# Kernel optimization log

Hardware: AMD Instinct MI355X
Metric: run time of the kernel (lower is better)

The kernel has to match this reference:

```python
import jax, jax.numpy as jnp
import numpy as np

B, T, D_MODEL = 1, 2048, 2048
N_HEADS, N_KV_HEADS, HEAD_DIM = 32, 8, 64
N_REP = N_HEADS // N_KV_HEADS
ROPE_THETA = 10000.0


def setup_inputs() -> dict:
    key = jax.random.key(0)
    ks = jax.random.split(key, 5)
    x = jax.random.normal(ks[0], (B, T, D_MODEL), dtype=jnp.float32)
    # rotary frequencies: complex exp stored as (cos, sin) pairs -> [T, HEAD_DIM//2, 2]
    inv_freq = 1.0 / (ROPE_THETA ** (jnp.arange(0, HEAD_DIM, 2, dtype=jnp.float32) / HEAD_DIM))
    angles = jnp.arange(T, dtype=jnp.float32)[:, None] * inv_freq[None, :]  # [T, HEAD_DIM//2]
    freqs_cis = jnp.stack([jnp.cos(angles), jnp.sin(angles)], axis=-1)  # [T, HD/2, 2]
    s = 1.0 / np.sqrt(D_MODEL)
    wq = jax.random.normal(ks[1], (D_MODEL, N_HEADS * HEAD_DIM), dtype=jnp.float32) * s
    wk = jax.random.normal(ks[2], (D_MODEL, N_KV_HEADS * HEAD_DIM), dtype=jnp.float32) * s
    wv = jax.random.normal(ks[3], (D_MODEL, N_KV_HEADS * HEAD_DIM), dtype=jnp.float32) * s
    wo = jax.random.normal(ks[4], (N_HEADS * HEAD_DIM, D_MODEL), dtype=jnp.float32) * (1.0 / np.sqrt(N_HEADS * HEAD_DIM))
    return {"x": x, "freqs_cis": freqs_cis, "wq": wq, "wk": wk, "wv": wv, "wo": wo}


def _apply_rotary(t, freqs_cis):
    # t: [B, T, H, D]; freqs_cis: [T, D//2, 2] as (cos, sin). Complex multiply.
    tr = t.astype(jnp.float32).reshape(*t.shape[:-1], -1, 2)  # [B,T,H,D/2,2]
    re, im = tr[..., 0], tr[..., 1]
    cos = freqs_cis[None, :, None, :, 0]  # [1,T,1,D/2]
    sin = freqs_cis[None, :, None, :, 1]
    out_re = re * cos - im * sin
    out_im = re * sin + im * cos
    out = jnp.stack([out_re, out_im], axis=-1).reshape(t.shape)
    return out.astype(t.dtype)


def reference(x, freqs_cis, wq, wk, wv, wo):
    Bx, Tx, _ = x.shape
    q = (x @ wq).reshape(Bx, Tx, N_HEADS, HEAD_DIM)
    k = (x @ wk).reshape(Bx, Tx, N_KV_HEADS, HEAD_DIM)
    v = (x @ wv).reshape(Bx, Tx, N_KV_HEADS, HEAD_DIM)
    q = _apply_rotary(q, freqs_cis)
    k = _apply_rotary(k, freqs_cis)
    # GQA: group query heads, broadcast against kv heads (no repeat materialization)
    qg = q.transpose(0, 2, 1, 3).reshape(Bx, N_KV_HEADS, N_REP, Tx, HEAD_DIM)  # [B,G,R,T,D]
    kg = k.transpose(0, 2, 1, 3)  # [B,G,T,D]
    vg = v.transpose(0, 2, 1, 3)  # [B,G,T,D]
    scale = 1.0 / np.sqrt(HEAD_DIM)
    scores = jnp.einsum('bgrtd,bgsd->bgrts', qg, kg) * scale  # [B,G,R,T,T]
    causal = jnp.tril(jnp.ones((Tx, Tx), dtype=bool))
    scores = jnp.where(causal, scores, jnp.finfo(scores.dtype).min)
    p = jax.nn.softmax(scores, axis=-1)
    y = jnp.einsum('bgrts,bgsd->bgrtd', p, vg)  # [B,G,R,T,D]
    y = y.reshape(Bx, N_HEADS, Tx, HEAD_DIM).transpose(0, 2, 1, 3).reshape(Bx, Tx, N_HEADS * HEAD_DIM)
    return y @ wo
```

## Files before the change

### kernel.cpp

```cpp
#include <hip/hip_runtime.h>
#include <hip/hip_bf16.h>
#include <stdint.h>
#include <stddef.h>

#define T_SEQ 2048
#define DMODEL 2048
#define NHEADS 32
#define NKV 8
#define HD 64
#define NQD (NHEADS * HD)
#define NKVD (NKV * HD)
#define QKVN (NQD + 2 * NKVD)

typedef __bf16 bf16_t;
typedef __bf16 bf16x8 __attribute__((ext_vector_type(8)));
typedef __bf16 bf16x4 __attribute__((ext_vector_type(4)));
typedef __bf16 bf16x2 __attribute__((ext_vector_type(2)));
typedef float f32x4 __attribute__((ext_vector_type(4)));

typedef __attribute__((address_space(1))) void gvoid_t;
typedef __attribute__((address_space(3))) void lvoid_t;

__device__ __forceinline__ void gload_lds16(const void* g, void* l) {
  __builtin_amdgcn_global_load_lds((gvoid_t*)g, (lvoid_t*)l, 16, 0, 0);
}

__global__ __launch_bounds__(256) void cast_f32_bf16_kernel(
    const float* __restrict__ in, bf16_t* __restrict__ out, int n8) {
  int i = blockIdx.x * 256 + threadIdx.x;
  if (i >= n8) return;
  const float4* p = (const float4*)in + (size_t)i * 2;
  float4 a = p[0], b = p[1];
  bf16x8 o = {(bf16_t)a.x, (bf16_t)a.y, (bf16_t)a.z, (bf16_t)a.w,
              (bf16_t)b.x, (bf16_t)b.y, (bf16_t)b.z, (bf16_t)b.w};
  *(bf16x8*)(out + (size_t)i * 8) = o;
}

__global__ __launch_bounds__(256) void transpose_cast_kernel(
    const float* __restrict__ in, bf16_t* __restrict__ out,
    int R, int C, int ldin, int ldout) {
  __shared__ float tile[32][33];
  const int c0 = blockIdx.x * 32, r0 = blockIdx.y * 32;
  const int tx = threadIdx.x & 31, ty = threadIdx.x >> 5;
#pragma unroll
  for (int i = 0; i < 32; i += 8)
    tile[ty + i][tx] = in[(size_t)(r0 + ty + i) * ldin + c0 + tx];
  __syncthreads();
#pragma unroll
  for (int i = 0; i < 32; i += 8)
    out[(size_t)(c0 + ty + i) * ldout + r0 + tx] = (bf16_t)tile[tx][ty + i];
}

__global__ __launch_bounds__(256) void rope_cast_kernel(
    const float* __restrict__ src, const float* __restrict__ fc,
    bf16_t* __restrict__ dst, int H, int ldin, float oscale) {
  const int i = blockIdx.x * 256 + threadIdx.x;
  const int npr = H * 32;
  const int t = i / npr;
  const int rem = i - t * npr;
  const int h = rem >> 5, fi = rem & 31;
  const float2 rein = *(const float2*)&src[(size_t)t * ldin + h * 64 + fi * 2];
  const float2 cs = *(const float2*)&fc[((size_t)t * 32 + fi) * 2];
  const float o0 = (rein.x * cs.x - rein.y * cs.y) * oscale;
  const float o1 = (rein.x * cs.y + rein.y * cs.x) * oscale;
  bf16x2 ob = {(bf16_t)o0, (bf16_t)o1};
  *(bf16x2*)&dst[(size_t)t * (H * 64) + h * 64 + fi * 2] = ob;
}

__global__ __launch_bounds__(256) void gemm_bt64_kernel(
    const bf16_t* __restrict__ A, const bf16_t* __restrict__ BT,
    float* __restrict__ C, int M, int N, int K) {
  __shared__ bf16_t As[128 * 64];
  __shared__ bf16_t Bs[64 * 64];
  const int tid = threadIdx.x;
  const int lane = tid & 63;
  const int w = tid >> 6;
  const int lr = lane & 15, lg = lane >> 4;
  const int m0 = blockIdx.y * 128, n0 = blockIdx.x * 64;
  const int wm = (w >> 1) * 64, wn = (w & 1) * 32;

  const bf16_t* gA[4];
  bf16_t* lA[4];
#pragma unroll
  for (int j = 0; j < 4; ++j) {
    const int c = tid + j * 256;
    const int row = c >> 3, cc = c & 7;
    gA[j] = A + (size_t)(m0 + row) * K + ((cc ^ (row & 7)) * 8);
    lA[j] = As + c * 8;
  }
  const bf16_t* gB[2];
  bf16_t* lB[2];
#pragma unroll
  for (int j = 0; j < 2; ++j) {
    const int c = tid + j * 256;
    const int row = c >> 3, cc = c & 7;
    gB[j] = BT + (size_t)(n0 + row) * K + ((cc ^ (row & 7)) * 8);
    lB[j] = Bs + c * 8;
  }

  f32x4 acc[4][2] = {};

  for (int k0 = 0; k0 < K; k0 += 64) {
#pragma unroll
    for (int j = 0; j < 4; ++j) gload_lds16(gA[j] + k0, lA[j]);
#pragma unroll
    for (int j = 0; j < 2; ++j) gload_lds16(gB[j] + k0, lB[j]);
    __syncthreads();
#pragma unroll
    for (int ks = 0; ks < 2; ++ks) {
      bf16x8 af[4], bfr[2];
#pragma unroll
      for (int mi = 0; mi < 4; ++mi) {
        const int row = wm + mi * 16 + lr;
        af[mi] = *(const bf16x8*)((const char*)As + row * 128 +
                                  ((ks * 64 + lg * 16) ^ ((row & 7) << 4)));
      }
#pragma unroll
      for (int nj = 0; nj < 2; ++nj) {
        const int row = wn + nj * 16 + lr;
        bfr[nj] = *(const bf16x8*)((const char*)Bs + row * 128 +
                                   ((ks * 64 + lg * 16) ^ ((row & 7) << 4)));
      }
      __builtin_amdgcn_s_setprio(1);
#pragma unroll
      for (int mi = 0; mi < 4; ++mi)
#pragma unroll
        for (int nj = 0; nj < 2; ++nj)
          acc[mi][nj] = __builtin_amdgcn_mfma_f32_16x16x32_bf16(
              af[mi], bfr[nj], acc[mi][nj], 0, 0, 0);
      __builtin_amdgcn_s_setprio(0);
    }
    __syncthreads();
  }

#pragma unroll
  for (int mi = 0; mi < 4; ++mi)
#pragma unroll
    for (int nj = 0; nj < 2; ++nj) {
      const int row = m0 + wm + mi * 16 + lg * 4;
      const int col = n0 + wn + nj * 16 + lr;
#pragma unroll
      for (int r = 0; r < 4; ++r)
        C[(size_t)(row + r) * N + col] = acc[mi][nj][r];
    }
}

__global__ __launch_bounds__(256) void attn_kernel(
    const bf16_t* __restrict__ Q, const bf16_t* __restrict__ Kb,
    const bf16_t* __restrict__ VT, bf16_t* __restrict__ Y,
    bf16_t* __restrict__ Yp, float* __restrict__ Mb, float* __restrict__ Lb) {
  __shared__ bf16_t Ks[2][64 * 64];
  __shared__ char Pb[4][32 * 128];
  const int bid = blockIdx.x;
  const int kh = bid & 7;
  const int item = bid >> 3;
  int qt, c, nc;
  if (item < 75) { qt = 63 - item / 3; c = item % 3; nc = 3; }
  else if (item < 115) { const int j = item - 75; qt = 38 - (j >> 1); c = j & 1; nc = 2; }
  else { qt = 18 - (item - 115); c = 0; nc = 1; }
  const int nt = (qt + 2) >> 1;
  const int tstart = (nt * c) / nc;
  const int tend = (nt * (c + 1)) / nc;
  const bool single = (nc == 1);

  const int tid = threadIdx.x, lane = tid & 63, w = tid >> 6;
  const int h = kh * 4 + w;
  const int lr = lane & 15, lg = lane >> 4;
  const int q0 = qt * 32;
  char* pb = (char*)Pb[w];
  const int swz = (lr & 7) << 4;

  const int r1 = tid >> 3, cc1 = tid & 7;
  const int r2 = r1 + 32;
  const bf16_t* kg1 = Kb + (size_t)r1 * NKVD + kh * HD + ((cc1 ^ (r1 & 7)) * 8);
  const bf16_t* kg2 = Kb + (size_t)r2 * NKVD + kh * HD + ((cc1 ^ (r2 & 7)) * 8);
  const int ld1 = tid * 8, ld2 = tid * 8 + 2048;
  const size_t kstep = (size_t)64 * NKVD;

  const bf16_t* vp0 = VT + (size_t)(kh * HD + 0 + lr) * T_SEQ + lg * 8 + tstart * 64;
  const bf16_t* vp1 = VT + (size_t)(kh * HD + 16 + lr) * T_SEQ + lg * 8 + tstart * 64;
  const bf16_t* vp2 = VT + (size_t)(kh * HD + 32 + lr) * T_SEQ + lg * 8 + tstart * 64;
  const bf16_t* vp3 = VT + (size_t)(kh * HD + 48 + lr) * T_SEQ + lg * 8 + tstart * 64;

  bf16x8 qf[2][2];
#pragma unroll
  for (int iq = 0; iq < 2; ++iq)
#pragma unroll
    for (int ks = 0; ks < 2; ++ks)
      qf[iq][ks] = *(const bf16x8*)&Q[(size_t)(q0 + iq * 16 + lr) * NQD + h * HD + ks * 32 + lg * 8];

  float m_i[2] = {-1e30f, -1e30f}, l_i[2] = {0.f, 0.f};
  f32x4 acc_o[2][4] = {};
  const f32x4 Z = {0.f, 0.f, 0.f, 0.f};

  size_t koff = (size_t)tstart * kstep;
  gload_lds16(kg1 + koff, &Ks[0][ld1]);
  gload_lds16(kg2 + koff, &Ks[0][ld2]);
  __syncthreads();

  int cur = 0;
  for (int t = tstart; t < tend; ++t) {
    const int s0 = t * 64;
    if (t + 1 < tend) {
      gload_lds16(kg1 + koff + kstep, &Ks[cur ^ 1][ld1]);
      gload_lds16(kg2 + koff + kstep, &Ks[cur ^ 1][ld2]);
    }
    koff += kstep;

    bf16x8 vf[2][4];
#pragma unroll
    for (int ks = 0; ks < 2; ++ks) {
      vf[ks][0] = *(const bf16x8*)(vp0 + ks * 32);
      vf[ks][1] = *(const bf16x8*)(vp1 + ks * 32);
      vf[ks][2] = *(const bf16x8*)(vp2 + ks * 32);
      vf[ks][3] = *(const bf16x8*)(vp3 + ks * 32);
    }
    vp0 += 64; vp1 += 64; vp2 += 64; vp3 += 64;

    const char* kbase = (const char*)&Ks[cur][0];
    bf16x8 kf[4][2];
#pragma unroll
    for (int j = 0; j < 4; ++j)
#pragma unroll
      for (int ks = 0; ks < 2; ++ks)
        kf[j][ks] = *(const bf16x8*)(kbase + (j * 16 + lr) * 128 + ((ks * 64 + lg * 16) ^ swz));

    f32x4 st[2][4];
    __builtin_amdgcn_s_setprio(1);
#pragma unroll
    for (int iq = 0; iq < 2; ++iq)
#pragma unroll
      for (int j = 0; j < 4; ++j) {
        st[iq][j] = __builtin_amdgcn_mfma_f32_16x16x32_bf16(kf[j][0], qf[iq][0], Z, 0, 0, 0);
        st[iq][j] = __builtin_amdgcn_mfma_f32_16x16x32_bf16(kf[j][1], qf[iq][1], st[iq][j], 0, 0, 0);
      }
    __builtin_amdgcn_s_setprio(0);

    const bool domask = (s0 + 64 > q0);
#pragma unroll
    for (int iq = 0; iq < 2; ++iq) {
      float sv[16];
      const int tq = q0 + iq * 16 + lr;
#pragma unroll
      for (int j = 0; j < 4; ++j)
#pragma unroll
        for (int r = 0; r < 4; ++r) {
          float v = st[iq][j][r];
          if (domask && (s0 + j * 16 + lg * 4 + r > tq)) v = -1e30f;
          sv[j * 4 + r] = v;
        }
      float pm = fmaxf(fmaxf(fmaxf(sv[0], sv[1]), fmaxf(sv[2], sv[3])),
                       fmaxf(fmaxf(sv[4], sv[5]), fmaxf(sv[6], sv[7])));
      float pm2 = fmaxf(fmaxf(fmaxf(sv[8], sv[9]), fmaxf(sv[10], sv[11])),
                        fmaxf(fmaxf(sv[12], sv[13]), fmaxf(sv[14], sv[15])));
      pm = fmaxf(pm, pm2);
      pm = fmaxf(pm, __shfl_xor(pm, 16));
      pm = fmaxf(pm, __shfl_xor(pm, 32));

      if (!__all(pm <= m_i[iq] + 8.0f)) {
        const float mnew = fmaxf(m_i[iq], pm);
        const float es = exp2f(m_i[iq] - mnew);
        m_i[iq] = mnew;
        l_i[iq] *= es;
        float eso[4];
#pragma unroll
        for (int r = 0; r < 4; ++r) eso[r] = __shfl(es, lg * 4 + r);
#pragma unroll
        for (int df = 0; df < 4; ++df)
#pragma unroll
          for (int r = 0; r < 4; ++r) acc_o[iq][df][r] *= eso[r];
      }

      float rs0 = 0.f, rs1 = 0.f;
      bf16_t pe[16];
#pragma unroll
      for (int z = 0; z < 8; ++z) {
        const float p = exp2f(sv[z] - m_i[iq]);
        rs0 += p;
        pe[z] = (bf16_t)p;
      }
#pragma unroll
      for (int z = 8; z < 16; ++z) {
        const float p = exp2f(sv[z] - m_i[iq]);
        rs1 += p;
        pe[z] = (bf16_t)p;
      }
      l_i[iq] += rs0 + rs1;

#pragma unroll
      for (int j = 0; j < 4; ++j) {
        bf16x4 pk = {pe[j * 4 + 0], pe[j * 4 + 1], pe[j * 4 + 2], pe[j * 4 + 3]};
        *(bf16x4*)(pb + (iq * 16 + lr) * 128 + ((j * 32 + lg * 8) ^ swz)) = pk;
      }
    }

    bf16x8 pa[2][2];
#pragma unroll
    for (int iq = 0; iq < 2; ++iq)
#pragma unroll
      for (int ks = 0; ks < 2; ++ks)
        pa[iq][ks] = *(const bf16x8*)(pb + (iq * 16 + lr) * 128 + ((ks * 64 + lg * 16) ^ swz));

    __builtin_amdgcn_s_setprio(1);
#pragma unroll
    for (int iq = 0; iq < 2; ++iq)
#pragma unroll
      for (int df = 0; df < 4; ++df)
#pragma unroll
        for (int ks = 0; ks < 2; ++ks)
          acc_o[iq][df] = __builtin_amdgcn_mfma_f32_16x16x32_bf16(pa[iq][ks], vf[ks][df], acc_o[iq][df], 0, 0, 0);
    __builtin_amdgcn_s_setprio(0);

    __syncthreads();
    cur ^= 1;
  }

  float lts[2];
#pragma unroll
  for (int iq = 0; iq < 2; ++iq) {
    float lt = l_i[iq];
    lt += __shfl_xor(lt, 16);
    lt += __shfl_xor(lt, 32);
    lts[iq] = lt;
  }
  if (single) {
#pragma unroll
    for (int iq = 0; iq < 2; ++iq) {
      float lf[4];
#pragma unroll
      for (int r = 0; r < 4; ++r) lf[r] = __shfl(lts[iq], lg * 4 + r);
#pragma unroll
      for (int r = 0; r < 4; ++r) {
        const float inv = 1.f / lf[r];
        const int t = q0 + iq * 16 + lg * 4 + r;
#pragma unroll
        for (int df = 0; df < 4; ++df)
          Y[(size_t)t * NQD + h * HD + df * 16 + lr] = (bf16_t)(acc_o[iq][df][r] * inv);
      }
    }
  } else {
    const int cid = (nc == 3) ? (kh * 115 + 40 + (qt - 39) * 3 + c)
                              : (kh * 115 + (qt - 19) * 2 + c);
    bf16_t* yp = Yp + ((size_t)cid * 4 + w) * 2048;
#pragma unroll
    for (int iq = 0; iq < 2; ++iq) {
      float lf[4];
#pragma unroll
      for (int r = 0; r < 4; ++r) lf[r] = __shfl(lts[iq], lg * 4 + r);
#pragma unroll
      for (int r = 0; r < 4; ++r) {
        const float inv = 1.f / lf[r];
        const int q = iq * 16 + lg * 4 + r;
#pragma unroll
        for (int df = 0; df < 4; ++df)
          yp[q * 64 + df * 16 + lr] = (bf16_t)(acc_o[iq][df][r] * inv);
      }
    }
    if (lg == 0) {
#pragma unroll
      for (int iq = 0; iq < 2; ++iq) {
        Mb[cid * 128 + w * 32 + iq * 16 + lr] = m_i[iq];
        Lb[cid * 128 + w * 32 + iq * 16 + lr] = lts[iq];
      }
    }
  }
}

__global__ __launch_bounds__(256) void merge_kernel(
    const bf16_t* __restrict__ Yp, const float* __restrict__ Mb,
    const float* __restrict__ Lb, bf16_t* __restrict__ Y) {
  const int qt = 19 + blockIdx.x, kh = blockIdx.y;
  const int w = threadIdx.x >> 6, lane = threadIdx.x & 63;
  const int h = kh * 4 + w;
  const int nc = (qt < 39) ? 2 : 3;
  const int base = (qt < 39) ? (kh * 115 + (qt - 19) * 2)
                             : (kh * 115 + 40 + (qt - 39) * 3);
  const bf16_t* y0 = Yp + ((size_t)(base + 0) * 4 + w) * 2048;
  const bf16_t* y1 = Yp + ((size_t)(base + 1) * 4 + w) * 2048;
  const bf16_t* y2 = Yp + ((size_t)(base + 2) * 4 + w) * 2048;
#pragma unroll 4
  for (int q = 0; q < 32; ++q) {
    const float m0 = Mb[(base + 0) * 128 + w * 32 + q];
    const float m1 = Mb[(base + 1) * 128 + w * 32 + q];
    const float l0 = Lb[(base + 0) * 128 + w * 32 + q];
    const float l1 = Lb[(base + 1) * 128 + w * 32 + q];
    float m2 = -1e30f, l2 = 0.f;
    if (nc == 3) {
      m2 = Mb[(base + 2) * 128 + w * 32 + q];
      l2 = Lb[(base + 2) * 128 + w * 32 + q];
    }
    const float M = fmaxf(fmaxf(m0, m1), m2);
    const float a0 = exp2f(m0 - M) * l0;
    const float a1 = exp2f(m1 - M) * l1;
    const float a2 = (nc == 3) ? exp2f(m2 - M) * l2 : 0.f;
    const float inv = 1.f / (a0 + a1 + a2);
    float v = (float)y0[q * 64 + lane] * a0 + (float)y1[q * 64 + lane] * a1;
    if (nc == 3) v += (float)y2[q * 64 + lane] * a2;
    Y[(size_t)(qt * 32 + q) * NQD + h * HD + lane] = (bf16_t)(v * inv);
  }
}

extern "C" void kernel_launch(void* const* d_in, const int* in_sizes, int n_in,
                              void* d_out, int out_size, void* d_ws, size_t ws_size,
                              hipStream_t stream) {
  const float* x = (const float*)d_in[0];
  const float* fc = (const float*)d_in[1];
  const float* wq = (const float*)d_in[2];
  const float* wk = (const float*)d_in[3];
  const float* wv = (const float*)d_in[4];
  const float* wo = (const float*)d_in[5];
  float* out = (float*)d_out;
  char* ws = (char*)d_ws;

  bf16_t* xb   = (bf16_t*)(ws + 0);
  bf16_t* wT   = (bf16_t*)(ws + (8u << 20));
  float*  qkvf = (float*)(ws + (20u << 20));
  bf16_t* qb   = (bf16_t*)(ws + (8u << 20));
  bf16_t* kb   = (bf16_t*)(ws + (16u << 20));
  bf16_t* vt   = (bf16_t*)(ws + (18u << 20));
  bf16_t* woT  = (bf16_t*)(ws + (20u << 20));
  bf16_t* yb   = (bf16_t*)(ws + 0);
  float*  Mb   = (float*)(ws + (28u << 20));
  float*  Lb   = (float*)(ws + (29u << 20));
  bf16_t* Yp   = (bf16_t*)d_out;

  const float SCL_Q = 0.18033688011112042f;

  hipLaunchKernelGGL(cast_f32_bf16_kernel, dim3(2048), dim3(256), 0, stream,
                     x, xb, (T_SEQ * DMODEL) / 8);
  hipLaunchKernelGGL(transpose_cast_kernel, dim3(64, 64), dim3(256), 0, stream,
                     wq, wT, DMODEL, NQD, NQD, DMODEL);
  hipLaunchKernelGGL(transpose_cast_kernel, dim3(16, 64), dim3(256), 0, stream,
                     wk, wT + (size_t)NQD * DMODEL, DMODEL, NKVD, NKVD, DMODEL);
  hipLaunchKernelGGL(transpose_cast_kernel, dim3(16, 64), dim3(256), 0, stream,
                     wv, wT + (size_t)(NQD + NKVD) * DMODEL, DMODEL, NKVD, NKVD, DMODEL);
  hipLaunchKernelGGL(gemm_bt64_kernel, dim3(QKVN / 64, T_SEQ / 128), dim3(256), 0, stream,
                     xb, wT, qkvf, T_SEQ, QKVN, DMODEL);
  hipLaunchKernelGGL(rope_cast_kernel, dim3((T_SEQ * NHEADS * 32) / 256), dim3(256), 0, stream,
                     qkvf, fc, qb, NHEADS, QKVN, SCL_Q);
  hipLaunchKernelGGL(rope_cast_kernel, dim3((T_SEQ * NKV * 32) / 256), dim3(256), 0, stream,
                     qkvf + NQD, fc, kb, NKV, QKVN, 1.0f);
  hipLaunchKernelGGL(transpose_cast_kernel, dim3(16, 64), dim3(256), 0, stream,
                     qkvf + NQD + NKVD, vt, T_SEQ, NKVD, QKVN, T_SEQ);
  hipLaunchKernelGGL(transpose_cast_kernel, dim3(64, 64), dim3(256), 0, stream,
                     wo, woT, NQD, DMODEL, DMODEL, NQD);
  hipLaunchKernelGGL(attn_kernel, dim3(134 * 8), dim3(256), 0, stream,
                     qb, kb, vt, yb, Yp, Mb, Lb);
  hipLaunchKernelGGL(merge_kernel, dim3(45, 8), dim3(256), 0, stream,
                     Yp, Mb, Lb, yb);
  hipLaunchKernelGGL(gemm_bt64_kernel, dim3(DMODEL / 64, T_SEQ / 128), dim3(256), 0, stream,
                     yb, woT, out, T_SEQ, DMODEL, NQD);
}
```

Baseline: 196.6 us.

## Double-buffer GEMM LDS tiles and interleave P readback in attention

The projection GEMM now uses two LDS buffers for A and B. It prefetches the next K-tile with global_load_lds while MFMAs run on the current tile, so each iteration needs one barrier instead of two. This is meant to hide global-load latency behind compute, at the cost of doubling shared memory to 48KB per block, which may lower occupancy. In the attention kernel, the P fragment readback from LDS moves inside the per-iq softmax loop, so the loads for one row group can overlap the softmax of the next.

```diff
diff --git a/kernel.cpp b/kernel.cpp
--- a/kernel.cpp
+++ b/kernel.cpp
@@ -70,8 +70,8 @@
 __global__ __launch_bounds__(256) void gemm_bt64_kernel(
     const bf16_t* __restrict__ A, const bf16_t* __restrict__ BT,
     float* __restrict__ C, int M, int N, int K) {
-  __shared__ bf16_t As[128 * 64];
-  __shared__ bf16_t Bs[64 * 64];
+  __shared__ bf16_t As[2][128 * 64];
+  __shared__ bf16_t Bs[2][64 * 64];
   const int tid = threadIdx.x;
   const int lane = tid & 63;
   const int w = tid >> 6;
@@ -80,45 +80,55 @@
   const int wm = (w >> 1) * 64, wn = (w & 1) * 32;
 
   const bf16_t* gA[4];
-  bf16_t* lA[4];
+  int lAo[4];
 #pragma unroll
   for (int j = 0; j < 4; ++j) {
     const int c = tid + j * 256;
     const int row = c >> 3, cc = c & 7;
     gA[j] = A + (size_t)(m0 + row) * K + ((cc ^ (row & 7)) * 8);
-    lA[j] = As + c * 8;
+    lAo[j] = c * 8;
   }
   const bf16_t* gB[2];
-  bf16_t* lB[2];
+  int lBo[2];
 #pragma unroll
   for (int j = 0; j < 2; ++j) {
     const int c = tid + j * 256;
     const int row = c >> 3, cc = c & 7;
     gB[j] = BT + (size_t)(n0 + row) * K + ((cc ^ (row & 7)) * 8);
-    lB[j] = Bs + c * 8;
+    lBo[j] = c * 8;
   }
 
   f32x4 acc[4][2] = {};
 
+#pragma unroll
+  for (int j = 0; j < 4; ++j) gload_lds16(gA[j], &As[0][lAo[j]]);
+#pragma unroll
+  for (int j = 0; j < 2; ++j) gload_lds16(gB[j], &Bs[0][lBo[j]]);
+  __syncthreads();
+
+  int cur = 0;
   for (int k0 = 0; k0 < K; k0 += 64) {
-#pragma unroll
-    for (int j = 0; j < 4; ++j) gload_lds16(gA[j] + k0, lA[j]);
-#pragma unroll
-    for (int j = 0; j < 2; ++j) gload_lds16(gB[j] + k0, lB[j]);
-    __syncthreads();
+    if (k0 + 64 < K) {
+#pragma unroll
+      for (int j = 0; j < 4; ++j) gload_lds16(gA[j] + k0 + 64, &As[cur ^ 1][lAo[j]]);
+#pragma unroll
+      for (int j = 0; j < 2; ++j) gload_lds16(gB[j] + k0 + 64, &Bs[cur ^ 1][lBo[j]]);
+    }
+    const char* Ab = (const char*)&As[cur][0];
+    const char* Bb = (const char*)&Bs[cur][0];
 #pragma unroll
     for (int ks = 0; ks < 2; ++ks) {
       bf16x8 af[4], bfr[2];
 #pragma unroll
       for (int mi = 0; mi < 4; ++mi) {
         const int row = wm + mi * 16 + lr;
-        af[mi] = *(const bf16x8*)((const char*)As + row * 128 +
+        af[mi] = *(const bf16x8*)(Ab + row * 128 +
                                   ((ks * 64 + lg * 16) ^ ((row & 7) << 4)));
       }
 #pragma unroll
       for (int nj = 0; nj < 2; ++nj) {
         const int row = wn + nj * 16 + lr;
-        bfr[nj] = *(const bf16x8*)((const char*)Bs + row * 128 +
+        bfr[nj] = *(const bf16x8*)(Bb + row * 128 +
                                    ((ks * 64 + lg * 16) ^ ((row & 7) << 4)));
       }
       __builtin_amdgcn_s_setprio(1);
@@ -131,6 +141,7 @@
       __builtin_amdgcn_s_setprio(0);
     }
     __syncthreads();
+    cur ^= 1;
   }
 
 #pragma unroll
@@ -237,6 +248,7 @@
     __builtin_amdgcn_s_setprio(0);
 
     const bool domask = (s0 + 64 > q0);
+    bf16x8 pa[2][2];
 #pragma unroll
     for (int iq = 0; iq < 2; ++iq) {
       float sv[16];
@@ -292,14 +304,10 @@
         bf16x4 pk = {pe[j * 4 + 0], pe[j * 4 + 1], pe[j * 4 + 2], pe[j * 4 + 3]};
         *(bf16x4*)(pb + (iq * 16 + lr) * 128 + ((j * 32 + lg * 8) ^ swz)) = pk;
       }
-    }
-
-    bf16x8 pa[2][2];
-#pragma unroll
-    for (int iq = 0; iq < 2; ++iq)
 #pragma unroll
       for (int ks = 0; ks < 2; ++ks)
         pa[iq][ks] = *(const bf16x8*)(pb + (iq * 16 + lr) * 128 + ((ks * 64 + lg * 16) ^ swz));
+    }
 
     __builtin_amdgcn_s_setprio(1);
 #pragma unroll
```

Result: faster. 191.4 us (-2.6%).
